# Performance work log

Hardware: AMD Instinct MI355X
Metric: run time of the kernel (lower is better)

Reference implementation:

```python
import jax, jax.numpy as jnp
import numpy as np

DEPTH = 4  # truncation depth of the signature


def setup_inputs() -> dict:
    key = jax.random.key(0)
    # (N, L, C) batch of paths
    path = jax.random.normal(key, (32, 256, 8), dtype=jnp.float32)
    return {"path": path}


def _signature(path, depth):
    """Truncated path signature via Chen's relation over linear segments.

    For a linear segment with increment dx, its signature is exp(dx) in the
    tensor algebra: level j = dx^{\otimes j} / j!.  The signature of the
    concatenated path is the tensor-algebra product of segment signatures,
    computed with a scan over segments.
    """
    N, L, C = path.shape
    dx = path[:, 1:, :] - path[:, :-1, :]  # (N, L-1, C) increments

    def exp_levels(d):
        # levels of exp(d): e_j = d^{\otimes j} / j!, flattened to (N, C^j)
        levels = [d]
        for j in range(2, depth + 1):
            nxt = jnp.einsum('na,nb->nab', levels[-1], d).reshape(N, -1) / j
            levels.append(nxt)
        return levels

    def step(carry, d):
        # carry: tuple of (N, C^k) for k = 1..depth (levels of running signature)
        # Chen: new_k = sum_{i+j=k} carry_i (x) e_j, with carry_0 = e_0 = 1
        e = exp_levels(d)
        new = []
        for k in range(1, depth + 1):
            acc = carry[k - 1] + e[k - 1]  # i=k,j=0 and i=0,j=k terms
            for i in range(1, k):
                acc = acc + jnp.einsum(
                    'na,nb->nab', carry[i - 1], e[k - i - 1]
                ).reshape(N, -1)
            new.append(acc)
        return tuple(new), None

    init = tuple(jnp.zeros((N, C ** k), path.dtype) for k in range(1, depth + 1))
    final, _ = jax.lax.scan(step, init, jnp.swapaxes(dx, 0, 1))  # scan over L-1
    return jnp.concatenate(final, axis=-1)  # (N, C + C^2 + ... + C^depth)


def reference(path):
    return _signature(path, DEPTH)
```

## Files before the change

### kernel.cpp

```cpp
#include <hip/hip_runtime.h>

#define NBATCH 32
#define LPATH 256
#define NSEG 255
#define SIGLEN 4680
#define PIMG 4712
#define PSTRF 4720
#define INV6 (1.0f/6.0f)
#define INV24 (1.0f/24.0f)

typedef float v2f __attribute__((ext_vector_type(2)));
typedef unsigned long long u64;
typedef unsigned int u32;

struct __align__(16) CBuf {
    float T4t2[4096];
    float T3b[544];
    float T2[64];
    float T1[8];
};

__device__ __forceinline__ void publish_half(CBuf& B, const v2f S4v[16],
                                             const float S3[4], float S2, float a1a,
                                             int l, int a, int b, int h) {
    #pragma unroll
    for (int ci = 0; ci < 4; ++ci)
        #pragma unroll
        for (int eh = 0; eh < 4; ++eh)
            *(v2f*)&B.T4t2[((4*h + ci)*4 + eh)*128 + 2*l] = S4v[ci*4 + eh];
    #pragma unroll
    for (int ci = 0; ci < 4; ++ci)
        B.T3b[a*68 + b*8 + 4*h + ci] = S3[ci];
    if (h == 0) {
        B.T2[l] = S2;
        if (b == 0) B.T1[a] = a1a;
    }
}

__device__ __forceinline__ void absorb_half(const CBuf& B, v2f S4v[16], float S3[4],
                                            float& S2, float& a1a,
                                            int l, int a, int b, int h) {
    v2f t1v[4];
    #pragma unroll
    for (int eh = 0; eh < 4; ++eh) t1v[eh] = *(const v2f*)&B.T1[2*eh];
    const float t1a = B.T1[a], t1b = B.T1[b];
    const v2f S2v = S2, a1v = a1a;
    #pragma unroll
    for (int ci = 0; ci < 4; ++ci) {
        const int c = 4*h + ci;
        const v2f S3cv = S3[ci];
        #pragma unroll
        for (int eh = 0; eh < 4; ++eh) {
            const v2f t2v = *(const v2f*)&B.T2[c*8 + 2*eh];
            const v2f t3v = *(const v2f*)&B.T3b[b*68 + c*8 + 2*eh];
            const v2f t4v = *(const v2f*)&B.T4t2[(c*4 + eh)*128 + 2*l];
            v2f acc = S4v[ci*4 + eh] + t4v;
            acc = __builtin_elementwise_fma(S3cv, t1v[eh], acc);
            acc = __builtin_elementwise_fma(S2v, t2v, acc);
            acc = __builtin_elementwise_fma(a1v, t3v, acc);
            S4v[ci*4 + eh] = acc;
        }
    }
    #pragma unroll
    for (int ci = 0; ci < 4; ++ci) {
        const int c = 4*h + ci;
        S3[ci] += S2 * B.T1[c] + a1a * B.T2[b*8 + c] + B.T3b[a*68 + b*8 + c];
    }
    S2 += a1a * t1b + B.T2[l];
    a1a += t1a;
}

__global__ __launch_bounds__(512)
__attribute__((amdgpu_waves_per_eu(2, 2)))
void sig_kernel(const float* __restrict__ path, float* __restrict__ pbase,
                int* __restrict__ flags, float* __restrict__ out) {
    const int blk = blockIdx.x;
    const int n = blk >> 1, cb = blk & 1;
    const int t = threadIdx.x;
    const int w = t >> 6, l = t & 63, a = l >> 3, b = l & 7;
    const int pr = w >> 1, h = w & 1;

    __shared__ CBuf bufs[4];
    __shared__ float dbuf[1024];
    __shared__ int sh_old;

    const float* prow = path + n * (LPATH*8);
    {
        const int i2 = t * 2;
        const int g2 = cb * 1024 + i2;
        v2f val = {0.f, 0.f};
        if (g2 + 1 < NSEG*8) {
            val.x = prow[g2 + 8] - prow[g2];
            val.y = prow[g2 + 9] - prow[g2 + 1];
        }
        *(v2f*)&dbuf[i2] = val;
    }
    __syncthreads();

    v2f S4v[16];
    float S3[4];
    #pragma unroll
    for (int j = 0; j < 16; ++j) S4v[j] = (v2f)0.f;
    #pragma unroll
    for (int ci = 0; ci < 4; ++ci) S3[ci] = 0.f;
    float S2 = 0.f, a1a = 0.f;

    const float* wbase = &dbuf[pr << 8];
    const float* abase = wbase + a;
    const float* bbase = wbase + b;

    #pragma unroll
    for (int ss = 0; ss < 32; ++ss) {
        const float4 dlo = *(const float4*)&wbase[ss*8];
        const float4 dhi = *(const float4*)&wbase[ss*8 + 4];
        const v2f dp0 = {dlo.x, dlo.y}, dp1 = {dlo.z, dlo.w};
        const v2f dp2 = {dhi.x, dhi.y}, dp3 = {dhi.z, dhi.w};
        const v2f dcl = h ? dp2 : dp0;
        const v2f dch = h ? dp3 : dp1;
        const float da = abase[ss*8];
        const float db = bbase[ss*8];
        const float dab = da * db;
        const float P = dab*INV24 + a1a*db*INV6 + S2*0.5f;
        const float Q = dab*INV6  + a1a*db*0.5f + S2;
        const v2f Pv = P, Qv = Q;
        v2f K0, K1;
        {
            v2f s3l = {S3[0], S3[1]};
            K0 = __builtin_elementwise_fma(dcl, Pv, s3l);
            s3l = __builtin_elementwise_fma(dcl, Qv, s3l);
            S3[0] = s3l.x; S3[1] = s3l.y;
        }
        {
            v2f s3h = {S3[2], S3[3]};
            K1 = __builtin_elementwise_fma(dch, Pv, s3h);
            s3h = __builtin_elementwise_fma(dch, Qv, s3h);
            S3[2] = s3h.x; S3[3] = s3h.y;
        }
        const float Kc[4] = {K0.x, K0.y, K1.x, K1.y};
        #pragma unroll
        for (int ci = 0; ci < 4; ++ci) {
            const v2f Kcv = Kc[ci];
            S4v[ci*4+0] = __builtin_elementwise_fma(dp0, Kcv, S4v[ci*4+0]);
            S4v[ci*4+1] = __builtin_elementwise_fma(dp1, Kcv, S4v[ci*4+1]);
            S4v[ci*4+2] = __builtin_elementwise_fma(dp2, Kcv, S4v[ci*4+2]);
            S4v[ci*4+3] = __builtin_elementwise_fma(dp3, Kcv, S4v[ci*4+3]);
        }
        S2 += db * (da*0.5f + a1a);
        a1a += da;
    }

    if (pr & 1) publish_half(bufs[pr >> 1], S4v, S3, S2, a1a, l, a, b, h);
    __syncthreads();
    if (!(pr & 1)) absorb_half(bufs[pr >> 1], S4v, S3, S2, a1a, l, a, b, h);
    __syncthreads();
    if (pr == 2) publish_half(bufs[0], S4v, S3, S2, a1a, l, a, b, h);
    __syncthreads();
    if (pr == 0) absorb_half(bufs[0], S4v, S3, S2, a1a, l, a, b, h);
    __syncthreads();

    if (pr == 0) {
        float* p = pbase + (size_t)blk * PSTRF;
        #pragma unroll
        for (int ci = 0; ci < 4; ++ci)
            #pragma unroll
            for (int eh = 0; eh < 4; ++eh) {
                u64 uv; __builtin_memcpy(&uv, &S4v[ci*4 + eh], 8);
                __hip_atomic_store((u64*)&p[((4*h + ci)*4 + eh)*128 + 2*l], uv,
                                   __ATOMIC_RELAXED, __HIP_MEMORY_SCOPE_AGENT);
            }
        #pragma unroll
        for (int ci = 0; ci < 4; ++ci) {
            u32 uv; __builtin_memcpy(&uv, &S3[ci], 4);
            __hip_atomic_store((u32*)&p[4096 + a*68 + b*8 + 4*h + ci], uv,
                               __ATOMIC_RELAXED, __HIP_MEMORY_SCOPE_AGENT);
        }
        if (h == 0) {
            u32 uv; __builtin_memcpy(&uv, &S2, 4);
            __hip_atomic_store((u32*)&p[4640 + l], uv,
                               __ATOMIC_RELAXED, __HIP_MEMORY_SCOPE_AGENT);
            if (b == 0) {
                u32 u1; __builtin_memcpy(&u1, &a1a, 4);
                __hip_atomic_store((u32*)&p[4704 + a], u1,
                                   __ATOMIC_RELAXED, __HIP_MEMORY_SCOPE_AGENT);
            }
        }
        asm volatile("s_waitcnt vmcnt(0)" ::: "memory");
    }
    __syncthreads();
    if (t == 0)
        sh_old = __hip_atomic_fetch_add(&flags[n], 1, __ATOMIC_RELAXED,
                                        __HIP_MEMORY_SCOPE_AGENT);
    __syncthreads();
    if (sh_old != 1) return;

    {
        const u64* src = (const u64*)(pbase + (size_t)(n*2 + (cb ^ 1)) * PSTRF);
        u64* dst = (u64*)&bufs[2];
        for (int i = t; i < PIMG/2; i += 512)
            dst[i] = __hip_atomic_load(&src[i], __ATOMIC_RELAXED,
                                       __HIP_MEMORY_SCOPE_AGENT);
    }
    __syncthreads();

    if (cb == 1) {
        if (pr == 0) publish_half(bufs[3], S4v, S3, S2, a1a, l, a, b, h);
        __syncthreads();
        if (pr == 0) {
            #pragma unroll
            for (int ci = 0; ci < 4; ++ci)
                #pragma unroll
                for (int eh = 0; eh < 4; ++eh)
                    S4v[ci*4 + eh] =
                        *(const v2f*)&bufs[2].T4t2[((4*h + ci)*4 + eh)*128 + 2*l];
            #pragma unroll
            for (int ci = 0; ci < 4; ++ci)
                S3[ci] = bufs[2].T3b[a*68 + b*8 + 4*h + ci];
            S2 = bufs[2].T2[l];
            a1a = bufs[2].T1[a];
            absorb_half(bufs[3], S4v, S3, S2, a1a, l, a, b, h);
        }
    } else {
        if (pr == 0) absorb_half(bufs[2], S4v, S3, S2, a1a, l, a, b, h);
    }

    if (pr == 0) {
        float* o = out + n * SIGLEN;
        if (h == 0) {
            if (b == 0) o[a] = a1a;
            o[8 + l] = S2;
        }
        *(float4*)&o[72 + l*8 + 4*h] = make_float4(S3[0], S3[1], S3[2], S3[3]);
        #pragma unroll
        for (int ci = 0; ci < 4; ++ci)
            #pragma unroll
            for (int eh = 0; eh < 4; ++eh)
                *(v2f*)&o[584 + l*64 + (4*h + ci)*8 + 2*eh] = S4v[ci*4 + eh];
    }
}

extern "C" void kernel_launch(void* const* d_in, const int* in_sizes, int n_in,
                              void* d_out, int out_size, void* d_ws, size_t ws_size,
                              hipStream_t stream) {
    const float* path = (const float*)d_in[0];
    float* out = (float*)d_out;
    int* flags = (int*)d_ws;
    float* pbase = (float*)d_ws + 256;
    hipMemsetAsync(d_ws, 0, NBATCH * sizeof(int), stream);
    sig_kernel<<<NBATCH * 2, 512, 0, stream>>>(path, pbase, flags, out);
}
```

Baseline: 21.42 us.

## Split each path across eight blocks and merge partial signatures with a tree reduction

Each batch element is now handled by eight workgroups instead of two, so every block scans only 32 segments (8 steps per wave pair) instead of 128. The last block to arrive loads the seven other partial signatures, from global memory into registers and LDS. It then combines them with a log-depth Chen-product tree across its four wave pairs. This shortens the serial scan and uses more CUs. In exchange it adds more global partial writes, more merge stages with block barriers, and more shared-memory buffers per block.

```diff
diff --git a/kernel.cpp b/kernel.cpp
--- a/kernel.cpp
+++ b/kernel.cpp
@@ -75,25 +75,27 @@
 void sig_kernel(const float* __restrict__ path, float* __restrict__ pbase,
                 int* __restrict__ flags, float* __restrict__ out) {
     const int blk = blockIdx.x;
-    const int n = blk >> 1, cb = blk & 1;
+    const int n = blk >> 3, cb = blk & 7;
     const int t = threadIdx.x;
     const int w = t >> 6, l = t & 63, a = l >> 3, b = l & 7;
     const int pr = w >> 1, h = w & 1;
 
-    __shared__ CBuf bufs[4];
-    __shared__ float dbuf[1024];
+    __shared__ CBuf bufs[6];
+    __shared__ float dbuf[256];
     __shared__ int sh_old;
 
     const float* prow = path + n * (LPATH*8);
-    {
-        const int i2 = t * 2;
-        const int g2 = cb * 1024 + i2;
-        v2f val = {0.f, 0.f};
-        if (g2 + 1 < NSEG*8) {
-            val.x = prow[g2 + 8] - prow[g2];
-            val.y = prow[g2 + 9] - prow[g2 + 1];
-        }
-        *(v2f*)&dbuf[i2] = val;
+    if (t < 64) {
+        const int i4 = t * 4;
+        const int g4 = cb * 256 + i4;
+        if (g4 < NSEG*8) {
+            const float4 x0 = *(const float4*)&prow[g4];
+            const float4 x1 = *(const float4*)&prow[g4 + 8];
+            *(float4*)&dbuf[i4] = make_float4(x1.x - x0.x, x1.y - x0.y,
+                                              x1.z - x0.z, x1.w - x0.w);
+        } else {
+            *(float4*)&dbuf[i4] = make_float4(0.f, 0.f, 0.f, 0.f);
+        }
     }
     __syncthreads();
 
@@ -105,12 +107,12 @@
     for (int ci = 0; ci < 4; ++ci) S3[ci] = 0.f;
     float S2 = 0.f, a1a = 0.f;
 
-    const float* wbase = &dbuf[pr << 8];
+    const float* wbase = &dbuf[pr << 6];
     const float* abase = wbase + a;
     const float* bbase = wbase + b;
 
     #pragma unroll
-    for (int ss = 0; ss < 32; ++ss) {
+    for (int ss = 0; ss < 8; ++ss) {
         const float4 dlo = *(const float4*)&wbase[ss*8];
         const float4 dhi = *(const float4*)&wbase[ss*8 + 4];
         const v2f dp0 = {dlo.x, dlo.y}, dp1 = {dlo.z, dlo.w};
@@ -191,37 +193,55 @@
         sh_old = __hip_atomic_fetch_add(&flags[n], 1, __ATOMIC_RELAXED,
                                         __HIP_MEMORY_SCOPE_AGENT);
     __syncthreads();
-    if (sh_old != 1) return;
+    if (sh_old != 7) return;
 
     {
-        const u64* src = (const u64*)(pbase + (size_t)(n*2 + (cb ^ 1)) * PSTRF);
-        u64* dst = (u64*)&bufs[2];
-        for (int i = t; i < PIMG/2; i += 512)
+        const u64* src = (const u64*)(pbase + (size_t)(n*8 + 2*pr + 1) * PSTRF);
+        u64* dst = (u64*)&bufs[2 + pr];
+        const int lt = t & 127;
+        for (int i = lt; i < PIMG/2; i += 128)
             dst[i] = __hip_atomic_load(&src[i], __ATOMIC_RELAXED,
                                        __HIP_MEMORY_SCOPE_AGENT);
-    }
-    __syncthreads();
-
-    if (cb == 1) {
-        if (pr == 0) publish_half(bufs[3], S4v, S3, S2, a1a, l, a, b, h);
-        __syncthreads();
-        if (pr == 0) {
+        const float* pimg = pbase + (size_t)(n*8 + 2*pr) * PSTRF;
+        #pragma unroll
+        for (int ci = 0; ci < 4; ++ci)
             #pragma unroll
-            for (int ci = 0; ci < 4; ++ci)
-                #pragma unroll
-                for (int eh = 0; eh < 4; ++eh)
-                    S4v[ci*4 + eh] =
-                        *(const v2f*)&bufs[2].T4t2[((4*h + ci)*4 + eh)*128 + 2*l];
-            #pragma unroll
-            for (int ci = 0; ci < 4; ++ci)
-                S3[ci] = bufs[2].T3b[a*68 + b*8 + 4*h + ci];
-            S2 = bufs[2].T2[l];
-            a1a = bufs[2].T1[a];
-            absorb_half(bufs[3], S4v, S3, S2, a1a, l, a, b, h);
-        }
-    } else {
-        if (pr == 0) absorb_half(bufs[2], S4v, S3, S2, a1a, l, a, b, h);
-    }
+            for (int eh = 0; eh < 4; ++eh) {
+                u64 uv = __hip_atomic_load(
+                    (const u64*)&pimg[((4*h + ci)*4 + eh)*128 + 2*l],
+                    __ATOMIC_RELAXED, __HIP_MEMORY_SCOPE_AGENT);
+                __builtin_memcpy(&S4v[ci*4 + eh], &uv, 8);
+            }
+        #pragma unroll
+        for (int ci = 0; ci < 4; ++ci) {
+            u32 uv = __hip_atomic_load(
+                (const u32*)&pimg[4096 + a*68 + b*8 + 4*h + ci],
+                __ATOMIC_RELAXED, __HIP_MEMORY_SCOPE_AGENT);
+            __builtin_memcpy(&S3[ci], &uv, 4);
+        }
+        {
+            u32 uv = __hip_atomic_load((const u32*)&pimg[4640 + l],
+                                       __ATOMIC_RELAXED, __HIP_MEMORY_SCOPE_AGENT);
+            __builtin_memcpy(&S2, &uv, 4);
+        }
+        {
+            u32 uv = __hip_atomic_load((const u32*)&pimg[4704 + a],
+                                       __ATOMIC_RELAXED, __HIP_MEMORY_SCOPE_AGENT);
+            __builtin_memcpy(&a1a, &uv, 4);
+        }
+    }
+    __syncthreads();
+
+    absorb_half(bufs[2 + pr], S4v, S3, S2, a1a, l, a, b, h);
+    __syncthreads();
+
+    if (pr & 1) publish_half(bufs[pr >> 1], S4v, S3, S2, a1a, l, a, b, h);
+    __syncthreads();
+    if (!(pr & 1)) absorb_half(bufs[pr >> 1], S4v, S3, S2, a1a, l, a, b, h);
+    __syncthreads();
+    if (pr == 2) publish_half(bufs[0], S4v, S3, S2, a1a, l, a, b, h);
+    __syncthreads();
+    if (pr == 0) absorb_half(bufs[0], S4v, S3, S2, a1a, l, a, b, h);
 
     if (pr == 0) {
         float* o = out + n * SIGLEN;
@@ -246,5 +266,5 @@
     int* flags = (int*)d_ws;
     float* pbase = (float*)d_ws + 256;
     hipMemsetAsync(d_ws, 0, NBATCH * sizeof(int), stream);
-    sig_kernel<<<NBATCH * 2, 512, 0, stream>>>(path, pbase, flags, out);
-}
+    sig_kernel<<<NBATCH * 8, 512, 0, stream>>>(path, pbase, flags, out);
+}
```

After: 28.07 us. 1.31x slower.
